# Performance work log

Measured on AMD Instinct MI355X. Metric: run time of the kernel, lower is better.

Reference implementation:

```python
import jax, jax.numpy as jnp
import numpy as np

H = 64  # hidden_size

def _lstm_layer(x, Wih, Whh, bih, bhh):
    # x: [B,T,I]; Wih: [4H,I]; Whh: [4H,H]; biases: [4H]
    # PyTorch gate order: i, f, g, o
    xg = jnp.einsum('bti,gi->btg', x, Wih) + (bih + bhh)  # [B,T,4H]
    B = x.shape[0]
    h0 = jnp.zeros((B, H), x.dtype)
    c0 = jnp.zeros((B, H), x.dtype)

    def step(carry, xg_t):
        h, c = carry
        gates = xg_t + h @ Whh.T  # [B,4H]
        i, f, g, o = jnp.split(gates, 4, axis=-1)
        i = jax.nn.sigmoid(i)
        f = jax.nn.sigmoid(f)
        g = jnp.tanh(g)
        o = jax.nn.sigmoid(o)
        c = f * c + i * g
        h = o * jnp.tanh(c)
        return (h, c), h

    _, hs = jax.lax.scan(step, (h0, c0), jnp.swapaxes(xg, 0, 1))  # hs: [T,B,H]
    return jnp.swapaxes(hs, 0, 1)  # [B,T,H]


def setup_inputs() -> dict:
    key = jax.random.key(0)
    ks = jax.random.split(key, 13)
    B, T, I = 1024, 512, 32
    s = 0.1
    return {
        'x': jax.random.normal(ks[0], (B, T, I), jnp.float32),
        'Wih0': jax.random.normal(ks[1], (4 * H, I), jnp.float32) * s,
        'Whh0': jax.random.normal(ks[2], (4 * H, H), jnp.float32) * s,
        'bih0': jax.random.normal(ks[3], (4 * H,), jnp.float32) * s,
        'bhh0': jax.random.normal(ks[4], (4 * H,), jnp.float32) * s,
        'Wih1': jax.random.normal(ks[5], (4 * H, H), jnp.float32) * s,
        'Whh1': jax.random.normal(ks[6], (4 * H, H), jnp.float32) * s,
        'bih1': jax.random.normal(ks[7], (4 * H,), jnp.float32) * s,
        'bhh1': jax.random.normal(ks[8], (4 * H,), jnp.float32) * s,
        'fc1_w': jax.random.normal(ks[9], (32, H), jnp.float32) * s,
        'fc1_b': jax.random.normal(ks[10], (32,), jnp.float32) * s,
        'fc2_w': jax.random.normal(ks[11], (2, 32), jnp.float32) * s,
        'fc2_b': jax.random.normal(ks[12], (2,), jnp.float32) * s,
    }


def reference(x, Wih0, Whh0, bih0, bhh0, Wih1, Whh1, bih1, bhh1, fc1_w, fc1_b, fc2_w, fc2_b):
    # Inference mode: dropout layers are identity.
    h1 = _lstm_layer(x, Wih0, Whh0, bih0, bhh0)   # [B,T,H]
    h2 = _lstm_layer(h1, Wih1, Whh1, bih1, bhh1)  # [B,T,H]
    h = h2[:, -1, :]                               # [B,H]
    z = jax.nn.relu(h @ fc1_w.T + fc1_b)           # [B,32]
    return z @ fc2_w.T + fc2_b                     # [B,2]
```

## Files before the change

### kernel.cpp

```cpp
#include <hip/hip_runtime.h>
#include <math.h>

#define TLEN 512
#define NB   1024
#define XSTR 48
#define HSTR 80
#define XLAY (4 * XSTR)
#define HLAY (4 * HSTR)

typedef _Float16 f16;
typedef f16   f16x4 __attribute__((ext_vector_type(4)));
typedef f16   f16x8 __attribute__((ext_vector_type(8)));
typedef float f32x4 __attribute__((ext_vector_type(4)));

__device__ __forceinline__ float sigf(float x) {
    return __builtin_amdgcn_rcpf(1.0f + __expf(-x));
}
__device__ __forceinline__ float tanhf_(float x) {
    return 2.0f * __builtin_amdgcn_rcpf(1.0f + __expf(-2.0f * x)) - 1.0f;
}
__device__ __forceinline__ float sel4(f32x4 v, int g) {
    float a = (g & 1) ? v[1] : v[0];
    float b = (g & 1) ? v[3] : v[2];
    return (g & 2) ? b : a;
}

__global__ __launch_bounds__(512, 2) void lstm_fused(
    const float* __restrict__ x,
    const float* __restrict__ Wih0, const float* __restrict__ Whh0,
    const float* __restrict__ bih0, const float* __restrict__ bhh0,
    const float* __restrict__ Wih1, const float* __restrict__ Whh1,
    const float* __restrict__ bih1, const float* __restrict__ bhh1,
    const float* __restrict__ fc1w, const float* __restrict__ fc1b,
    const float* __restrict__ fc2w, const float* __restrict__ fc2b,
    float* __restrict__ out)
{
    __shared__ __align__(16) f16 xbuf[2 * XLAY];
    __shared__ __align__(16) f16 h1buf[2 * HLAY];
    __shared__ __align__(16) f16 h2buf[2 * HLAY];
    __shared__ float zbuf[4][33];

    const int tid   = threadIdx.x;
    const int lane  = tid & 63;
    const int w     = tid >> 6;
    const int wg    = w & 3;
    const bool isL0 = (w < 4);
    const int bc    = lane & 15;
    const int lq    = lane >> 4;
    const int G     = bc >> 2;
    const int b_own = bc & 3;
    const int bg0   = blockIdx.x * 4;

    f16x8 A[4][4];
    float bsv[4];
    #pragma unroll
    for (int g = 0; g < 4; ++g) {
        const int gr = g * 64 + 16 * wg + bc;
        #pragma unroll
        for (int s = 0; s < 4; ++s) {
            #pragma unroll
            for (int i = 0; i < 8; ++i) {
                int k = 32 * s + lq * 8 + i;
                float v = 0.0f;
                if (isL0) {
                    if (s < 3) v = (k < 32) ? Wih0[gr * 32 + k] : Whh0[gr * 64 + (k - 32)];
                } else {
                    v = (k < 64) ? Wih1[gr * 64 + k] : Whh1[gr * 64 + (k - 64)];
                }
                A[g][s][i] = (f16)v;
            }
        }
        const int gd = g * 64 + 16 * wg + 4 * lq + G;
        bsv[g] = isL0 ? (bih0[gd] + bhh0[gd]) : (bih1[gd] + bhh1[gd]);
    }

    for (int i = tid; i < 2 * XLAY; i += 512) xbuf[i] = (f16)0;
    for (int i = tid; i < 2 * HLAY; i += 512) { h1buf[i] = (f16)0; h2buf[i] = (f16)0; }
    __syncthreads();

    const bool xduty = (w == 0) && (lane < 32);
    const int  xbat = lane >> 3, xchk = lane & 7;
    const float* xg = x + ((long)(bg0 + xbat) * TLEN) * 32 + xchk * 4;
    const int xw_off = xbat * XSTR + xchk * 4;
    float4 xpre;
    if (xduty) {
        float4 v = *(const float4*)xg;
        f16x4 h; h[0]=(f16)v.x; h[1]=(f16)v.y; h[2]=(f16)v.z; h[3]=(f16)v.w;
        *(f16x4*)(xbuf + xw_off) = h;
        xpre = *(const float4*)(xg + 32);
    }
    __syncthreads();

    const int bcx = b_own * XSTR + lq * 8;
    const int bch = b_own * HSTR + lq * 8;
    const int hwr = b_own * HSTR + 16 * wg + 4 * lq + G;

    float cst = 0.0f;

#define CELL_UPDATE(HBUF, PW)                                                 \
    {                                                                         \
        float pi = sel4(a0, G) + bsv[0];                                      \
        float pf = sel4(a1, G) + bsv[1];                                      \
        float pg = sel4(a2, G) + bsv[2];                                      \
        float po = sel4(a3, G) + bsv[3];                                      \
        float iv = sigf(pi), fv = sigf(pf);                                   \
        float gv = tanhf_(pg), ov = sigf(po);                                 \
        cst = fmaf(fv, cst, iv * gv);                                         \
        HBUF[(PW) * HLAY + hwr] = (f16)(ov * tanhf_(cst));                    \
    }

#define L0_PHASE(p, itv)                                                      \
    {                                                                         \
        f16x8 b0 = *(const f16x8*)(xbuf  + (p) * XLAY + bcx);                 \
        f16x8 b1 = *(const f16x8*)(h1buf + ((p)^1) * HLAY + bch);             \
        f16x8 b2 = *(const f16x8*)(h1buf + ((p)^1) * HLAY + bch + 32);        \
        f32x4 a0 = {0.f,0.f,0.f,0.f}, a1 = a0, a2 = a0, a3 = a0;              \
        a0 = __builtin_amdgcn_mfma_f32_16x16x32_f16(A[0][0], b0, a0, 0,0,0);  \
        a1 = __builtin_amdgcn_mfma_f32_16x16x32_f16(A[1][0], b0, a1, 0,0,0);  \
        a2 = __builtin_amdgcn_mfma_f32_16x16x32_f16(A[2][0], b0, a2, 0,0,0);  \
        a3 = __builtin_amdgcn_mfma_f32_16x16x32_f16(A[3][0], b0, a3, 0,0,0);  \
        a0 = __builtin_amdgcn_mfma_f32_16x16x32_f16(A[0][1], b1, a0, 0,0,0);  \
        a1 = __builtin_amdgcn_mfma_f32_16x16x32_f16(A[1][1], b1, a1, 0,0,0);  \
        a2 = __builtin_amdgcn_mfma_f32_16x16x32_f16(A[2][1], b1, a2, 0,0,0);  \
        a3 = __builtin_amdgcn_mfma_f32_16x16x32_f16(A[3][1], b1, a3, 0,0,0);  \
        a0 = __builtin_amdgcn_mfma_f32_16x16x32_f16(A[0][2], b2, a0, 0,0,0);  \
        a1 = __builtin_amdgcn_mfma_f32_16x16x32_f16(A[1][2], b2, a1, 0,0,0);  \
        a2 = __builtin_amdgcn_mfma_f32_16x16x32_f16(A[2][2], b2, a2, 0,0,0);  \
        a3 = __builtin_amdgcn_mfma_f32_16x16x32_f16(A[3][2], b2, a3, 0,0,0);  \
        if (xduty) {                   \
            f16x4 hx; hx[0]=(f16)xpre.x; hx[1]=(f16)xpre.y;                   \
            hx[2]=(f16)xpre.z; hx[3]=(f16)xpre.w;                             \
            *(f16x4*)(xbuf + ((p)^1) * XLAY + xw_off) = hx;                   \
            int tn = ((itv) + 2 < TLEN) ? (itv) + 2 : TLEN - 1;               \
            xpre = *(const float4*)(xg + (long)tn * 32);                      \
        }                                                                     \
        CELL_UPDATE(h1buf, p)                                                 \
    }

#define L1_PHASE(p)                                                           \
    {                                                                         \
        f16x8 b0 = *(const f16x8*)(h1buf + ((p)^1) * HLAY + bch);             \
        f16x8 b1 = *(const f16x8*)(h1buf + ((p)^1) * HLAY + bch + 32);        \
        f16x8 b2 = *(const f16x8*)(h2buf + (p) * HLAY + bch);                 \
        f16x8 b3 = *(const f16x8*)(h2buf + (p) * HLAY + bch + 32);            \
        f32x4 a0 = {0.f,0.f,0.f,0.f}, a1 = a0, a2 = a0, a3 = a0;              \
        a0 = __builtin_amdgcn_mfma_f32_16x16x32_f16(A[0][0], b0, a0, 0,0,0);  \
        a1 = __builtin_amdgcn_mfma_f32_16x16x32_f16(A[1][0], b0, a1, 0,0,0);  \
        a2 = __builtin_amdgcn_mfma_f32_16x16x32_f16(A[2][0], b0, a2, 0,0,0);  \
        a3 = __builtin_amdgcn_mfma_f32_16x16x32_f16(A[3][0], b0, a3, 0,0,0);  \
        a0 = __builtin_amdgcn_mfma_f32_16x16x32_f16(A[0][1], b1, a0, 0,0,0);  \
        a1 = __builtin_amdgcn_mfma_f32_16x16x32_f16(A[1][1], b1, a1, 0,0,0);  \
        a2 = __builtin_amdgcn_mfma_f32_16x16x32_f16(A[2][1], b1, a2, 0,0,0);  \
        a3 = __builtin_amdgcn_mfma_f32_16x16x32_f16(A[3][1], b1, a3, 0,0,0);  \
        a0 = __builtin_amdgcn_mfma_f32_16x16x32_f16(A[0][2], b2, a0, 0,0,0);  \
        a1 = __builtin_amdgcn_mfma_f32_16x16x32_f16(A[1][2], b2, a1, 0,0,0);  \
        a2 = __builtin_amdgcn_mfma_f32_16x16x32_f16(A[2][2], b2, a2, 0,0,0);  \
        a3 = __builtin_amdgcn_mfma_f32_16x16x32_f16(A[3][2], b2, a3, 0,0,0);  \
        a0 = __builtin_amdgcn_mfma_f32_16x16x32_f16(A[0][3], b3, a0, 0,0,0);  \
        a1 = __builtin_amdgcn_mfma_f32_16x16x32_f16(A[1][3], b3, a1, 0,0,0);  \
        a2 = __builtin_amdgcn_mfma_f32_16x16x32_f16(A[2][3], b3, a2, 0,0,0);  \
        a3 = __builtin_amdgcn_mfma_f32_16x16x32_f16(A[3][3], b3, a3, 0,0,0);  \
        CELL_UPDATE(h2buf, (p)^1)                                             \
    }

    if (isL0) L0_PHASE(0, 0)
    __syncthreads();

    #pragma unroll 1
    for (int k = 0; k < 255; ++k) {
        if (isL0) L0_PHASE(1, 2 * k + 1) else L1_PHASE(1)
        __syncthreads();
        if (isL0) L0_PHASE(0, 2 * k + 2) else L1_PHASE(0)
        __syncthreads();
    }

    if (isL0) L0_PHASE(1, 511) else L1_PHASE(1)
    __syncthreads();
    if (!isL0) L1_PHASE(0)
    __syncthreads();

#undef L0_PHASE
#undef L1_PHASE
#undef CELL_UPDATE

    const f16* h2f = h2buf + HLAY;
    if (tid < 128) {
        int b = tid >> 5, m = tid & 31;
        float z = fc1b[m];
        #pragma unroll
        for (int j = 0; j < 64; ++j)
            z = fmaf(fc1w[m * 64 + j], (float)h2f[b * HSTR + j], z);
        zbuf[b][m] = fmaxf(z, 0.0f);
    }
    __syncthreads();
    if (tid < 8) {
        int b = tid >> 1, o = tid & 1;
        float s = fc2b[o];
        #pragma unroll
        for (int m = 0; m < 32; ++m)
            s = fmaf(fc2w[o * 32 + m], zbuf[b][m], s);
        out[(long)(bg0 + b) * 2 + o] = s;
    }
}

extern "C" void kernel_launch(void* const* d_in, const int* in_sizes, int n_in,
                              void* d_out, int out_size, void* d_ws, size_t ws_size,
                              hipStream_t stream) {
    const float* x    = (const float*)d_in[0];
    const float* Wih0 = (const float*)d_in[1];
    const float* Whh0 = (const float*)d_in[2];
    const float* bih0 = (const float*)d_in[3];
    const float* bhh0 = (const float*)d_in[4];
    const float* Wih1 = (const float*)d_in[5];
    const float* Whh1 = (const float*)d_in[6];
    const float* bih1 = (const float*)d_in[7];
    const float* bhh1 = (const float*)d_in[8];
    const float* fc1w = (const float*)d_in[9];
    const float* fc1b = (const float*)d_in[10];
    const float* fc2w = (const float*)d_in[11];
    const float* fc2b = (const float*)d_in[12];
    float* out = (float*)d_out;

    lstm_fused<<<dim3(NB / 4), dim3(512), 0, stream>>>(
        x, Wih0, Whh0, bih0, bhh0, Wih1, Whh1, bih1, bhh1,
        fc1w, fc1b, fc2w, fc2b, out);
}
```

Baseline: 242.9 us.

## Stage x in 64-step chunks via block-wide LDS refills

Replaces the per-step x prefetch, where half of wave 0 loads one timestep of x from global memory every phase, with double-buffered 64-timestep chunks loaded cooperatively by all 512 threads. Refills happen only once every 64 steps, so the global-load latency and the extra register traffic are taken off the per-step critical path of the layer-0 waves. In exchange LDS usage grows to roughly 33 KB for x, and each refill step briefly stalls all waves, including the layer-1 waves, at the barrier.

```diff
diff --git a/kernel.cpp b/kernel.cpp
--- a/kernel.cpp
+++ b/kernel.cpp
@@ -3,10 +3,11 @@
 
 #define TLEN 512
 #define NB   1024
-#define XSTR 48
 #define HSTR 80
-#define XLAY (4 * XSTR)
 #define HLAY (4 * HSTR)
+#define XCH  64
+#define XBSTR (XCH * 32 + 16)
+#define XHALF (4 * XBSTR)
 
 typedef _Float16 f16;
 typedef f16   f16x4 __attribute__((ext_vector_type(4)));
@@ -35,7 +36,7 @@
     const float* __restrict__ fc2w, const float* __restrict__ fc2b,
     float* __restrict__ out)
 {
-    __shared__ __align__(16) f16 xbuf[2 * XLAY];
+    __shared__ __align__(16) f16 x_lds[2 * XHALF];
     __shared__ __align__(16) f16 h1buf[2 * HLAY];
     __shared__ __align__(16) f16 h2buf[2 * HLAY];
     __shared__ float zbuf[4][33];
@@ -74,25 +75,35 @@
         bsv[g] = isL0 ? (bih0[gd] + bhh0[gd]) : (bih1[gd] + bhh1[gd]);
     }
 
-    for (int i = tid; i < 2 * XLAY; i += 512) xbuf[i] = (f16)0;
     for (int i = tid; i < 2 * HLAY; i += 512) { h1buf[i] = (f16)0; h2buf[i] = (f16)0; }
-    __syncthreads();
-
-    const bool xduty = (w == 0) && (lane < 32);
-    const int  xbat = lane >> 3, xchk = lane & 7;
-    const float* xg = x + ((long)(bg0 + xbat) * TLEN) * 32 + xchk * 4;
-    const int xw_off = xbat * XSTR + xchk * 4;
-    float4 xpre;
-    if (xduty) {
-        float4 v = *(const float4*)xg;
-        f16x4 h; h[0]=(f16)v.x; h[1]=(f16)v.y; h[2]=(f16)v.z; h[3]=(f16)v.w;
-        *(f16x4*)(xbuf + xw_off) = h;
-        xpre = *(const float4*)(xg + 32);
-    }
-    __syncthreads();
-
-    const int bcx = b_own * XSTR + lq * 8;
+
+    const int rf_b   = tid >> 7;
+    const int rf_rem = tid & 127;
+#define REFILL(ch)                                                            \
+    {                                                                         \
+        f16* dst = x_lds + ((ch) & 1) * XHALF + rf_b * XBSTR;                 \
+        const float4* src = (const float4*)(x +                               \
+            ((long)(bg0 + rf_b) * TLEN + (ch) * XCH) * 32);                   \
+        float4 v0 = src[rf_rem];                                              \
+        float4 v1 = src[rf_rem + 128];                                        \
+        float4 v2 = src[rf_rem + 256];                                        \
+        float4 v3 = src[rf_rem + 384];                                        \
+        f16x4 h;                                                              \
+        h[0]=(f16)v0.x; h[1]=(f16)v0.y; h[2]=(f16)v0.z; h[3]=(f16)v0.w;       \
+        *(f16x4*)(dst + (rf_rem)       * 4) = h;                              \
+        h[0]=(f16)v1.x; h[1]=(f16)v1.y; h[2]=(f16)v1.z; h[3]=(f16)v1.w;       \
+        *(f16x4*)(dst + (rf_rem + 128) * 4) = h;                              \
+        h[0]=(f16)v2.x; h[1]=(f16)v2.y; h[2]=(f16)v2.z; h[3]=(f16)v2.w;       \
+        *(f16x4*)(dst + (rf_rem + 256) * 4) = h;                              \
+        h[0]=(f16)v3.x; h[1]=(f16)v3.y; h[2]=(f16)v3.z; h[3]=(f16)v3.w;       \
+        *(f16x4*)(dst + (rf_rem + 384) * 4) = h;                              \
+    }
+
+    REFILL(0)
+    __syncthreads();
+
     const int bch = b_own * HSTR + lq * 8;
+    const int bxx = b_own * XBSTR + lq * 8;
     const int hwr = b_own * HSTR + 16 * wg + 4 * lq + G;
 
     float cst = 0.0f;
@@ -111,7 +122,8 @@
 
 #define L0_PHASE(p, itv)                                                      \
     {                                                                         \
-        f16x8 b0 = *(const f16x8*)(xbuf  + (p) * XLAY + bcx);                 \
+        f16x8 b0 = *(const f16x8*)(x_lds + (((itv) >> 6) & 1) * XHALF +       \
+                                   ((itv) & (XCH - 1)) * 32 + bxx);           \
         f16x8 b1 = *(const f16x8*)(h1buf + ((p)^1) * HLAY + bch);             \
         f16x8 b2 = *(const f16x8*)(h1buf + ((p)^1) * HLAY + bch + 32);        \
         f32x4 a0 = {0.f,0.f,0.f,0.f}, a1 = a0, a2 = a0, a3 = a0;              \
@@ -127,13 +139,6 @@
         a1 = __builtin_amdgcn_mfma_f32_16x16x32_f16(A[1][2], b2, a1, 0,0,0);  \
         a2 = __builtin_amdgcn_mfma_f32_16x16x32_f16(A[2][2], b2, a2, 0,0,0);  \
         a3 = __builtin_amdgcn_mfma_f32_16x16x32_f16(A[3][2], b2, a3, 0,0,0);  \
-        if (xduty) {                   \
-            f16x4 hx; hx[0]=(f16)xpre.x; hx[1]=(f16)xpre.y;                   \
-            hx[2]=(f16)xpre.z; hx[3]=(f16)xpre.w;                             \
-            *(f16x4*)(xbuf + ((p)^1) * XLAY + xw_off) = hx;                   \
-            int tn = ((itv) + 2 < TLEN) ? (itv) + 2 : TLEN - 1;               \
-            xpre = *(const float4*)(xg + (long)tn * 32);                      \
-        }                                                                     \
         CELL_UPDATE(h1buf, p)                                                 \
     }
 
@@ -164,13 +169,17 @@
     }
 
     if (isL0) L0_PHASE(0, 0)
+    REFILL(1)
     __syncthreads();
 
     #pragma unroll 1
     for (int k = 0; k < 255; ++k) {
         if (isL0) L0_PHASE(1, 2 * k + 1) else L1_PHASE(1)
         __syncthreads();
-        if (isL0) L0_PHASE(0, 2 * k + 2) else L1_PHASE(0)
+        const int it2 = 2 * k + 2;
+        if (isL0) L0_PHASE(0, it2) else L1_PHASE(0)
+        if ((it2 & (XCH - 1)) == 0 && it2 <= TLEN - 2 * XCH)
+            REFILL((it2 >> 6) + 1)
         __syncthreads();
     }
 
@@ -182,6 +191,7 @@
 #undef L0_PHASE
 #undef L1_PHASE
 #undef CELL_UPDATE
+#undef REFILL
 
     const f16* h2f = h2buf + HLAY;
     if (tid < 128) {
```

New measurement: 247.4 us. About the same (+1.9%).
